# Kernel optimization log

Hardware: AMD Instinct MI355X
Metric: run time of the kernel (lower is better)

Reference implementation:

```python
import jax, jax.numpy as jnp
import numpy as np

N_NODES = 50000
N_EDGES = 800000
IN_CH = 128
OUT_CH = 128
N_REL = 8
N_BASES = 8


def setup_inputs() -> dict:
    key = jax.random.key(0)
    ks = jax.random.split(key, 8)
    x = jax.random.normal(ks[0], (N_NODES, IN_CH), dtype=jnp.float32)
    edge_index = jax.random.randint(ks[1], (2, N_EDGES), 0, N_NODES, dtype=jnp.int64)
    edge_type = jax.random.randint(ks[2], (N_EDGES,), 0, N_REL, dtype=jnp.int64)
    # learned parameters (PyG RGCNConv basis decomposition + root + bias, PReLU alpha)
    scale = 1.0 / np.sqrt(IN_CH)
    basis = jax.random.normal(ks[3], (N_BASES, IN_CH, OUT_CH), dtype=jnp.float32) * scale
    comp = jax.random.normal(ks[4], (N_REL, N_BASES), dtype=jnp.float32) * (1.0 / np.sqrt(N_BASES))
    root = jax.random.normal(ks[5], (IN_CH, OUT_CH), dtype=jnp.float32) * scale
    bias = jnp.zeros((OUT_CH,), dtype=jnp.float32)
    alpha = jnp.full((OUT_CH,), 0.25, dtype=jnp.float32)  # PReLU per-channel weight
    return {"x": x, "edge_index": edge_index, "edge_type": edge_type,
            "basis": basis, "comp": comp, "root": root, "bias": bias, "alpha": alpha}


def reference(x, edge_index, edge_type, basis, comp, root, bias, alpha):
    N = x.shape[0]
    R = comp.shape[0]
    # basis decomposition: W_r = sum_b comp[r,b] * basis[b]   -> [R, in, out]
    W = jnp.einsum('rb,bio->rio', comp, basis)
    # transform every node under every relation once (cheaper than per-edge matmul)
    xw = jnp.einsum('ni,rio->rno', x, W)  # [R, N, out]
    src = edge_index[0]
    dst = edge_index[1]
    msg = xw[edge_type, src]  # [E, out] gather per edge
    # PyG RGCNConv default aggr='mean': mean over incoming edges PER relation
    seg = edge_type * N + dst  # combined (relation, dst) segment id
    cnt = jax.ops.segment_sum(jnp.ones(msg.shape[0], dtype=x.dtype), seg, num_segments=R * N)
    norm = 1.0 / jnp.maximum(cnt, 1.0)
    agg = jax.ops.segment_sum(msg * norm[seg][:, None], dst, num_segments=N)  # [N, out]
    out = agg + x @ root + bias
    # PReLU with per-channel alpha
    return jnp.where(out >= 0, out, alpha * out)
```

## Files before the change

### kernel.cpp

```cpp
#include <hip/hip_runtime.h>
#include <hip/hip_bf16.h>


#define N_NODES 50000
#define N_EDGES 800000
#define N_REL   8
#define CH      128
#define KTOT    1152
#define NSEG    (N_NODES * N_REL)
#define DT      16
#define SCAN_BLK 1024
#define NSCAN   ((NSEG + SCAN_BLK - 1) / SCAN_BLK)
#define BSTRIDE 1160
#define WBLK    576

typedef __attribute__((ext_vector_type(8))) short bf16x8;
typedef __attribute__((ext_vector_type(4))) float f32x4;

__global__ void k_prep(const float* __restrict__ basis, const float* __restrict__ comp,
                       const float* __restrict__ root, __hip_bfloat16* __restrict__ WcatT,
                       const float* __restrict__ x, unsigned int* __restrict__ xb) {
  int b = blockIdx.x, tid = threadIdx.x;
  if (b < WBLK) {
    int idx = b * 256 + tid;
    int o = idx / KTOT, k = idx % KTOT;
    float v;
    if (k < N_REL * CH) {
      int r = k >> 7, i = k & (CH - 1);
      float acc = 0.f;
#pragma unroll
      for (int bb = 0; bb < 8; ++bb) acc += comp[r * 8 + bb] * basis[(bb * CH + i) * CH + o];
      v = acc;
    } else {
      v = root[(k - N_REL * CH) * CH + o];
    }
    WcatT[(size_t)o * KTOT + k] = __float2bfloat16(v);
  } else {
    int idx = (b - WBLK) * 256 + tid;
    const float4 v = *reinterpret_cast<const float4*>(x + (size_t)idx * 4);
    __hip_bfloat16 h0 = __float2bfloat16(v.x), h1 = __float2bfloat16(v.y);
    __hip_bfloat16 h2 = __float2bfloat16(v.z), h3 = __float2bfloat16(v.w);
    xb[(size_t)idx * 2]     = *(unsigned short*)&h0 | ((unsigned int)*(unsigned short*)&h1 << 16);
    xb[(size_t)idx * 2 + 1] = *(unsigned short*)&h2 | ((unsigned int)*(unsigned short*)&h3 << 16);
  }
}

__global__ void k_hist(const int* __restrict__ dst, const int* __restrict__ et,
                       int* __restrict__ hist) {
  int e = blockIdx.x * 256 + threadIdx.x;
  if (e < N_EDGES) atomicAdd(&hist[dst[e] * N_REL + et[e]], 1);
}

__global__ void k_scan1(const int* __restrict__ hist, int* __restrict__ off,
                        int* __restrict__ bsum) {
  __shared__ int sd[256];
  int t = threadIdx.x, b = blockIdx.x;
  int base = b * SCAN_BLK + t * 4;
  int v[4]; int s = 0;
#pragma unroll
  for (int j = 0; j < 4; ++j) { int i = base + j; v[j] = (i < NSEG) ? hist[i] : 0; s += v[j]; }
  sd[t] = s; __syncthreads();
  for (int o = 1; o < 256; o <<= 1) {
    int add = (t >= o) ? sd[t - o] : 0; __syncthreads();
    sd[t] += add; __syncthreads();
  }
  int excl = sd[t] - s;
  int run = excl;
#pragma unroll
  for (int j = 0; j < 4; ++j) { int i = base + j; if (i < NSEG) off[i] = run; run += v[j]; }
  if (t == 255) bsum[b] = sd[255];
}

__global__ void k_scan2(int* __restrict__ bsum) {
  __shared__ int sd[512];
  int t = threadIdx.x;
  int v = (t < NSCAN) ? bsum[t] : 0;
  sd[t] = v; __syncthreads();
  for (int o = 1; o < 512; o <<= 1) {
    int add = (t >= o) ? sd[t - o] : 0; __syncthreads();
    sd[t] += add; __syncthreads();
  }
  int excl = (t == 0) ? 0 : sd[t - 1];
  if (t < NSCAN) bsum[t] = excl;
}

__global__ void k_scan3(int* __restrict__ off, const int* __restrict__ bsum) {
  int t = threadIdx.x, b = blockIdx.x;
  int add = bsum[b];
  int base = b * SCAN_BLK + t * 4;
#pragma unroll
  for (int j = 0; j < 4; ++j) { int i = base + j; if (i < NSEG) off[i] += add; }
}

__global__ void k_scatter(const int* __restrict__ src, const int* __restrict__ dst,
                          const int* __restrict__ et, int* __restrict__ off,
                          int* __restrict__ srcPk) {
  int e = blockIdx.x * 256 + threadIdx.x;
  if (e >= N_EDGES) return;
  int d = dst[e], r = et[e];
  int key = d * N_REL + r;
  int pos = atomicAdd(&off[key], 1);
  srcPk[pos] = src[e] | (r << 16) | ((d & 15) << 19);
}

__global__ __launch_bounds__(512)
void k_fused(const unsigned int* __restrict__ xb,
             const int* __restrict__ off, const int* __restrict__ srcPk,
             const __hip_bfloat16* __restrict__ WcatT,
             const float* __restrict__ bias, const float* __restrict__ alpha,
             float* __restrict__ out) {
  __shared__ __hip_bfloat16 B16[DT * BSTRIDE];
  __shared__ float invc[DT * N_REL];
  int tid = threadIdx.x;
  int wave = tid >> 6, lane = tid & 63;
  int dstBase = blockIdx.x * DT;
  int seg0 = dstBase * N_REL;

  for (int i = tid; i < DT * 128; i += 512) {
    int row = i >> 7, c = i & 127;
    *reinterpret_cast<int4*>(&B16[row * BSTRIDE + c * 8]) = make_int4(0, 0, 0, 0);
  }
  for (int i = tid; i < DT * 64; i += 512) {
    int row = i >> 6, c = i & 63;
    *reinterpret_cast<unsigned int*>(&B16[row * BSTRIDE + 1024 + c * 2]) =
        xb[(size_t)(dstBase + row) * 64 + c];
  }
  if (tid < DT * N_REL) {
    int sg = seg0 + tid;
    int beg = (sg == 0) ? 0 : off[sg - 1];
    int c = off[sg] - beg;
    invc[tid] = (c > 0) ? 1.0f / (float)c : 0.0f;
  }
  int segw = seg0 + wave * 16;
  int ebeg = (segw == 0) ? 0 : off[segw - 1];
  int eend = off[segw + 15];
  __syncthreads();

  float a0 = 0.f, a1 = 0.f;
  int curKey = -1;
  auto flush = [&]() {
    if (curKey >= 0) {
      int ld = curKey >> 3, r = curKey & 7;
      float iv = invc[(ld << 3) | r];
      __hip_bfloat16 b0 = __float2bfloat16(a0 * iv);
      __hip_bfloat16 b1 = __float2bfloat16(a1 * iv);
      unsigned int pk2 = (unsigned int)*(unsigned short*)&b0 |
                         ((unsigned int)*(unsigned short*)&b1 << 16);
      *reinterpret_cast<unsigned int*>(&B16[ld * BSTRIDE + r * CH + lane * 2]) = pk2;
    }
  };
  if (ebeg < eend) {
    int nb = (eend - ebeg + 15) >> 4;
    int l16 = lane & 15;
    int pklA = srcPk[min(ebeg + l16, eend - 1)];
    int pklB = srcPk[min(ebeg + 16 + l16, eend - 1)];
    for (int b = 0; b < nb; ++b) {
      int base = ebeg + b * 16;
      int pk[16];
#pragma unroll
      for (int j = 0; j < 16; ++j) pk[j] = __builtin_amdgcn_readlane(pklA, j);
      unsigned int u[16];
#pragma unroll
      for (int j = 0; j < 16; ++j)
        u[j] = xb[(size_t)(unsigned)(pk[j] & 0xFFFF) * 64 + lane];
      int pklC = srcPk[min(base + 32 + l16, eend - 1)];
#pragma unroll
      for (int j = 0; j < 16; ++j) {
        if (base + j < eend) {
          int key = pk[j] >> 16;
          if (key != curKey) { flush(); curKey = key; a0 = 0.f; a1 = 0.f; }
          a0 += __uint_as_float(u[j] << 16);
          a1 += __uint_as_float(u[j] & 0xffff0000u);
        }
      }
      pklA = pklB; pklB = pklC;
    }
    flush();
  }
  __syncthreads();

  int r16 = lane & 15, g = lane >> 4;
  f32x4 acc = {0.f, 0.f, 0.f, 0.f};
  const short* Wt = reinterpret_cast<const short*>(WcatT) + (size_t)(wave * 16 + r16) * KTOT;
  const short* Arow = reinterpret_cast<const short*>(B16) + r16 * BSTRIDE;
  for (int kk = 0; kk < KTOT / 32; ++kk) {
    int kb = kk * 32 + g * 8;
    bf16x8 af = *reinterpret_cast<const bf16x8*>(Arow + kb);
    bf16x8 bw = *reinterpret_cast<const bf16x8*>(Wt + kb);
    acc = __builtin_amdgcn_mfma_f32_16x16x32_bf16(af, bw, acc, 0, 0, 0);
  }

  int col = wave * 16 + r16;
  float bi = bias[col], al = alpha[col];
#pragma unroll
  for (int rg = 0; rg < 4; ++rg) {
    int row = g * 4 + rg;
    float v = acc[rg] + bi;
    v = (v >= 0.f) ? v : al * v;
    out[(size_t)(dstBase + row) * CH + col] = v;
  }
}

extern "C" void kernel_launch(void* const* d_in, const int* in_sizes, int n_in,
                              void* d_out, int out_size, void* d_ws, size_t ws_size,
                              hipStream_t stream) {
  const float* x     = (const float*)d_in[0];
  const int*   ei    = (const int*)d_in[1];
  const int*   etype = (const int*)d_in[2];
  const float* basis = (const float*)d_in[3];
  const float* comp  = (const float*)d_in[4];
  const float* root  = (const float*)d_in[5];
  const float* bias  = (const float*)d_in[6];
  const float* alpha = (const float*)d_in[7];
  const int* src = ei;
  const int* dst = ei + N_EDGES;
  float* out = (float*)d_out;

  char* ws = (char*)d_ws;
  size_t p = 0;
  auto alloc = [&](size_t bytes) {
    void* q = ws + p;
    p = (p + bytes + 255) & ~(size_t)255;
    return q;
  };
  __hip_bfloat16* WcatT = (__hip_bfloat16*)alloc((size_t)CH * KTOT * sizeof(__hip_bfloat16));
  int* off    = (int*)alloc((size_t)NSEG * sizeof(int));
  int* hist   = (int*)alloc((size_t)NSEG * sizeof(int));
  int* bsum   = (int*)alloc((size_t)NSCAN * sizeof(int));
  int* srcPk  = (int*)alloc((size_t)N_EDGES * sizeof(int));
  unsigned int* xb = (unsigned int*)alloc((size_t)N_NODES * CH / 2 * sizeof(unsigned int));

  hipMemsetAsync(hist, 0, (size_t)NSEG * sizeof(int), stream);
  k_prep<<<WBLK + N_NODES * CH / 4 / 256, 256, 0, stream>>>(basis, comp, root, WcatT, x, xb);
  k_hist<<<(N_EDGES + 255) / 256, 256, 0, stream>>>(dst, etype, hist);
  k_scan1<<<NSCAN, 256, 0, stream>>>(hist, off, bsum);
  k_scan2<<<1, 512, 0, stream>>>(bsum);
  k_scan3<<<NSCAN, 256, 0, stream>>>(off, bsum);
  k_scatter<<<(N_EDGES + 255) / 256, 256, 0, stream>>>(src, dst, etype, off, srcPk);
  k_fused<<<N_NODES / DT, 512, 0, stream>>>(xb, off, srcPk, WcatT, bias, alpha, out);
}
```

Baseline: 252.1 us.

## Stage neighbor feature gathers into LDS via global_load_lds double buffering

After: 292.1 us. 1.16x slower.

```diff
diff --git a/kernel.cpp b/kernel.cpp
--- a/kernel.cpp
+++ b/kernel.cpp
@@ -16,6 +16,8 @@
 
 typedef __attribute__((ext_vector_type(8))) short bf16x8;
 typedef __attribute__((ext_vector_type(4))) float f32x4;
+typedef const __attribute__((address_space(1))) unsigned int* gas_u32;
+typedef __attribute__((address_space(3))) unsigned int* las_u32;
 
 __global__ void k_prep(const float* __restrict__ basis, const float* __restrict__ comp,
                        const float* __restrict__ root, __hip_bfloat16* __restrict__ WcatT,
@@ -111,6 +113,7 @@
              float* __restrict__ out) {
   __shared__ __hip_bfloat16 B16[DT * BSTRIDE];
   __shared__ float invc[DT * N_REL];
+  __shared__ unsigned stageU[8 * 1024];
   int tid = threadIdx.x;
   int wave = tid >> 6, lane = tid & 63;
   int dstBase = blockIdx.x * DT;
@@ -150,30 +153,57 @@
     }
   };
   if (ebeg < eend) {
-    int nb = (eend - ebeg + 15) >> 4;
-    int l16 = lane & 15;
-    int pklA = srcPk[min(ebeg + l16, eend - 1)];
-    int pklB = srcPk[min(ebeg + 16 + l16, eend - 1)];
-    for (int b = 0; b < nb; ++b) {
-      int base = ebeg + b * 16;
-      int pk[16];
-#pragma unroll
-      for (int j = 0; j < 16; ++j) pk[j] = __builtin_amdgcn_readlane(pklA, j);
-      unsigned int u[16];
-#pragma unroll
-      for (int j = 0; j < 16; ++j)
-        u[j] = xb[(size_t)(unsigned)(pk[j] & 0xFFFF) * 64 + lane];
-      int pklC = srcPk[min(base + 32 + l16, eend - 1)];
-#pragma unroll
-      for (int j = 0; j < 16; ++j) {
-        if (base + j < eend) {
-          int key = pk[j] >> 16;
-          if (key != curKey) { flush(); curKey = key; a0 = 0.f; a1 = 0.f; }
-          a0 += __uint_as_float(u[j] << 16);
-          a1 += __uint_as_float(u[j] & 0xffff0000u);
+    unsigned* stW = &stageU[wave * 1024];
+    for (int sb = ebeg; sb < eend; sb += 64) {
+      int desc = srcPk[min(sb + lane, eend - 1)];
+      int m = min(64, eend - sb);
+      int nc = (m + 7) >> 3;
+#pragma unroll
+      for (int j = 0; j < 8; ++j) {
+        if (j < m) {
+          int pk = __builtin_amdgcn_readlane(desc, j);
+          __builtin_amdgcn_global_load_lds(
+              (gas_u32)(xb + (size_t)(unsigned)(pk & 0xFFFF) * 64 + lane),
+              (las_u32)(stW + j * 64), 4, 0, 0);
         }
       }
-      pklA = pklB; pklB = pklC;
+      __builtin_amdgcn_sched_barrier(0);
+      for (int c = 0; c < nc; ++c) {
+        int nxt = (c + 1) * 8;
+        bool haveNext = nxt < m;
+        bool nextFull = nxt + 8 <= m;
+        if (haveNext) {
+#pragma unroll
+          for (int j = 0; j < 8; ++j) {
+            if (nxt + j < m) {
+              int pk = __builtin_amdgcn_readlane(desc, nxt + j);
+              __builtin_amdgcn_global_load_lds(
+                  (gas_u32)(xb + (size_t)(unsigned)(pk & 0xFFFF) * 64 + lane),
+                  (las_u32)(stW + (((c + 1) & 1) * 8 + j) * 64), 4, 0, 0);
+            }
+          }
+        }
+        __builtin_amdgcn_sched_barrier(0);
+        if (haveNext && nextFull) {
+          asm volatile("s_waitcnt vmcnt(8)" ::: "memory");
+        } else {
+          asm volatile("s_waitcnt vmcnt(0)" ::: "memory");
+        }
+        __builtin_amdgcn_sched_barrier(0);
+#pragma unroll
+        for (int j = 0; j < 8; ++j) {
+          int e = c * 8 + j;
+          if (e < m) {
+            int pk = __builtin_amdgcn_readlane(desc, e);
+            unsigned u = stW[((c & 1) * 8 + j) * 64 + lane];
+            int key = pk >> 16;
+            if (key != curKey) { flush(); curKey = key; a0 = 0.f; a1 = 0.f; }
+            a0 += __uint_as_float(u << 16);
+            a1 += __uint_as_float(u & 0xffff0000u);
+          }
+        }
+        __builtin_amdgcn_sched_barrier(0);
+      }
     }
     flush();
   }
```
